# Kernel tuning notes

Hardware: AMD Instinct MI355X
Metric: run time of the kernel (lower is better)

Reference implementation:

```python
import jax, jax.numpy as jnp
import numpy as np

INV_SQRT3 = 0.5773502691896258  # e3nn wigner_3j entries for (0,1,1),(1,0,1),(1,1,0)


def setup_inputs() -> dict:
    key = jax.random.key(0)
    ks = jax.random.split(key, 9)
    B, N = 2, 256
    d_in, m1 = 256, 1          # input irreps: d_in x0e + m1 x1o
    d_h, m5, m3 = 256, 5, 3    # hidden irreps: d_h x0e + 5 x1o + 3 x1o
    d_out = 2                  # output irreps: 2 x0e
    return {
        "vectors": jax.random.normal(ks[0], (B, N, 3 * m1), jnp.float32),
        "scalars": jax.random.normal(ks[1], (B, N, d_in), jnp.float32),
        # e3nn internal weights ~ N(0,1); one weight block per CG path (uvw)
        "W1": jax.random.normal(ks[2], (d_in, d_in, d_h), jnp.float32),   # 0e x 0e -> 0e
        "W2a": jax.random.normal(ks[3], (d_in, m1, m5), jnp.float32),     # 0e x 1o -> 1o (mul 5)
        "W2b": jax.random.normal(ks[4], (d_in, m1, m3), jnp.float32),     # 0e x 1o -> 1o (mul 3)
        "W3a": jax.random.normal(ks[5], (m1, d_in, m5), jnp.float32),     # 1o x 0e -> 1o (mul 5)
        "W3b": jax.random.normal(ks[6], (m1, d_in, m3), jnp.float32),     # 1o x 0e -> 1o (mul 3)
        "W4": jax.random.normal(ks[7], (m1, m1, d_h), jnp.float32),       # 1o x 1o -> 0e
        "WL": jax.random.normal(ks[8], (d_h, d_out), jnp.float32),        # Linear d_h x0e -> 2 x0e
    }


def reference(vectors, scalars, W1, W2a, W2b, W3a, W3b, W4, WL):
    B, N, d = scalars.shape
    m1 = vectors.shape[-1] // 3
    z = B * N
    s = scalars.reshape(z, d)          # (z, d)  scalar (0e) channels
    v = vectors.reshape(z, m1, 3)      # (z, m1, 3)  vector (1o) channels
    d_h = W1.shape[-1]
    # e3nn FullyConnectedTensorProduct path weights ('component' irrep norm,
    # 'element' path norm): sqrt(ir_out.dim / sum_paths(mul1*mul2))
    pw0 = (1.0 / (d * d + m1 * m1)) ** 0.5      # into 0e output (paths 0e*0e and 1o*1o)
    pw1 = (3.0 / (2.0 * d * m1)) ** 0.5         # into each 1o output (paths 0e*1o and 1o*0e)
    # --- 0e x 0e -> 0e (dominant path) + 1o x 1o -> 0e ---
    t = jnp.einsum('zu,uvw->zvw', s, W1)        # (z, d, d_h)
    out0 = jnp.einsum('zv,zvw->zw', s, t)       # (z, d_h)
    out0 = out0 + INV_SQRT3 * jnp.einsum('zui,zvi,uvw->zw', v, v, W4)
    out0 = pw0 * out0
    # --- 0e x 1o -> 1o and 1o x 0e -> 1o (present in hidden irreps; they have
    # no path into the final 2x0e output, kept for structural fidelity) ---
    out1 = pw1 * INV_SQRT3 * (jnp.einsum('zu,zvk,uvw->zwk', s, v, W2a)
                              + jnp.einsum('zuk,zv,uvw->zwk', v, s, W3a))  # (z,5,3)
    out2 = pw1 * INV_SQRT3 * (jnp.einsum('zu,zvk,uvw->zwk', s, v, W2b)
                              + jnp.einsum('zuk,zv,uvw->zwk', v, s, W3b))  # (z,3,3)
    del out1, out2
    # --- e3nn Linear(hidden, 2x0e): only 0e->0e path, 1/sqrt(fan_in) norm ---
    lin = jnp.einsum('zu,uw->zw', out0, WL) / (d_h ** 0.5)   # (z, 2)
    m_eqv = lin[:, :1].reshape(B, N, 1)
    m_inv = lin[:, 1:].reshape(B, N, 1)
    return (m_eqv, m_inv)
```

## Files before the change

### kernel.cpp

```cpp
#include <hip/hip_runtime.h>


typedef __attribute__((ext_vector_type(8))) _Float16 f16x8;
typedef __attribute__((ext_vector_type(2))) _Float16 f16x2;
typedef __attribute__((ext_vector_type(4))) float f32x4;
typedef __attribute__((ext_vector_type(2))) int int2v;
typedef __attribute__((ext_vector_type(4))) int int4v;

#define LDS_S 32768
#define BP 80
#define BSTEP 5120
#define LDS_TOTAL (LDS_S + 4 * BSTEP)

__device__ __forceinline__ unsigned pkrtz(float a, float b) {
  return __builtin_bit_cast(unsigned, __builtin_amdgcn_cvt_pkrtz(a, b));
}
__device__ __forceinline__ int hbits(f16x2 h) {
  return __builtin_bit_cast(int, h);
}
__device__ __forceinline__ void barrier_lds() {
  asm volatile("s_waitcnt lgkmcnt(0)" ::: "memory");
  __builtin_amdgcn_s_barrier();
}

__global__ __launch_bounds__(256, 3) void eg_gemm(const float* __restrict__ s,
                                                  const float* __restrict__ W1,
                                                  float* __restrict__ out0) {
  extern __shared__ char smem[];
  char* sB = smem + LDS_S;

  const int bx = blockIdx.x;
  const int zh = bx >> 8;
  const int uvw = bx & 255;
  const int wt = uvw & 3, vc = (uvw >> 2) & 7, uc = uvw >> 5;
  const int u0 = uc * 32, v0 = vc * 32, w0 = wt * 64;

  const int t = threadIdx.x;
  const int lane = t & 63;
  const int wid = t >> 6;
  const int l15 = lane & 15;
  const int g = lane >> 4;

  for (int j = 0; j < 16; ++j) {
    int id = j * 256 + t;
    int zl = id >> 4;
    int c4 = id & 15;
    int srccol = (c4 < 8) ? (u0 + (c4 << 2)) : (v0 + ((c4 - 8) << 2));
    const float4 f = *(const float4*)(s + (zh * 256 + zl) * 256 + srccol);
    int slot = c4 >> 1;
    char* dst = smem + zl * 128 + (((slot ^ (zl & 7)) << 4) | ((c4 & 1) << 3));
    *(int2v*)dst = int2v{(int)pkrtz(f.x, f.y), (int)pkrtz(f.z, f.w)};
  }

  const int wB = t & 63;
  const int vg = t >> 6;
  const int hsw = (wB >> 3) & 7;
  const int sl0 = (vg ^ hsw) << 3;
  const int sl1 = ((vg + 4) ^ hsw) << 3;
  const float* gB = W1 + (size_t)u0 * 65536 + (v0 + vg * 4) * 256 + w0 + wB;

  float pa0, pa1, pa2, pa3, pa4, pa5, pa6, pa7;
  float pb0, pb1, pb2, pb3, pb4, pb5, pb6, pb7;

#define ISSUE(usbase)                                                       \
  do {                                                                      \
    const float* q0_ = gB + (size_t)(usbase) * 65536;                       \
    pa0 = q0_[0];    pa1 = q0_[256];      pa2 = q0_[512];  pa3 = q0_[768];  \
    pa4 = q0_[4096]; pa5 = q0_[4096+256]; pa6 = q0_[4096+512];              \
    pa7 = q0_[4096+768];                                                    \
    const float* q1_ = q0_ + 65536;                                         \
    pb0 = q1_[0];    pb1 = q1_[256];      pb2 = q1_[512];  pb3 = q1_[768];  \
    pb4 = q1_[4096]; pb5 = q1_[4096+256]; pb6 = q1_[4096+512];              \
    pb7 = q1_[4096+768];                                                    \
  } while (0)

#define WRITEPF(dst0_)                                                       \
  do {                                                                       \
    char* d0_ = (dst0_);                                                     \
    *(int2v*)(d0_ + wB * BP + sl0) =                                         \
        int2v{(int)pkrtz(pa0, pa1), (int)pkrtz(pa2, pa3)};                   \
    *(int2v*)(d0_ + wB * BP + sl1) =                                         \
        int2v{(int)pkrtz(pa4, pa5), (int)pkrtz(pa6, pa7)};                   \
    char* d1_ = d0_ + BSTEP;                                                 \
    *(int2v*)(d1_ + wB * BP + sl0) =                                         \
        int2v{(int)pkrtz(pb0, pb1), (int)pkrtz(pb2, pb3)};                   \
    *(int2v*)(d1_ + wB * BP + sl1) =                                         \
        int2v{(int)pkrtz(pb4, pb5), (int)pkrtz(pb6, pb7)};                   \
  } while (0)

  ISSUE(0);
  WRITEPF(sB);
  ISSUE(2);
  barrier_lds();

  const int swz = l15 & 7;
  int4v sv[4];
#pragma unroll
  for (int mf = 0; mf < 4; ++mf) {
    const char* p = smem + (wid * 64 + mf * 16 + l15) * 128 + (((4 + g) ^ swz) << 4);
    sv[mf] = *(const int4v*)p;
  }

  int baddr[4];
#pragma unroll
  for (int nf = 0; nf < 4; ++nf) {
    int w = nf * 16 + l15;
    baddr[nf] = w * BP + (((2 * g) ^ ((w >> 3) & 7)) << 3);
  }

  f32x4 acc[4][4];
#pragma unroll
  for (int a = 0; a < 4; ++a)
#pragma unroll
    for (int b = 0; b < 4; ++b) acc[a][b] = 0.f;

  for (int q = 0; q < 8; ++q) {
    int2v sur[4];
#pragma unroll
    for (int mf = 0; mf < 4; ++mf) {
      const char* p = smem + (wid * 64 + mf * 16 + l15) * 128 +
                      ((((q >> 1) ^ swz) << 4) | ((q & 1) << 3));
      sur[mf] = *(const int2v*)p;
    }
#pragma unroll
    for (int rr = 0; rr < 2; ++rr) {
      const int r = 2 * q + rr;
      const char* bufc = sB + rr * (2 * BSTEP);
      char* bufn = sB + (rr ^ 1) * (2 * BSTEP);
#pragma unroll
      for (int p = 0; p < 2; ++p) {
        f16x8 afr[4];
#pragma unroll
        for (int mf = 0; mf < 4; ++mf) {
          unsigned dw = (unsigned)sur[mf][rr];
          unsigned s2 = __builtin_amdgcn_perm(dw, dw, p ? 0x03020302u : 0x01000100u);
          f16x2 su2 = __builtin_bit_cast(f16x2, s2);
          int4v af;
#pragma unroll
          for (int jj = 0; jj < 4; ++jj) {
            f16x2 pv = __builtin_bit_cast(f16x2, (unsigned)sv[mf][jj]);
            f16x2 pr = su2 * pv;
            af[jj] = hbits(pr);
          }
          afr[mf] = __builtin_bit_cast(f16x8, af);
        }
        const char* bp = bufc + p * BSTEP;
#pragma unroll
        for (int nf = 0; nf < 4; ++nf) {
          int2v d0 = *(const int2v*)(bp + baddr[nf]);
          int2v d1 = *(const int2v*)(bp + (baddr[nf] ^ 8));
          int4v bf4 = int4v{d0[0], d0[1], d1[0], d1[1]};
          f16x8 bfr = __builtin_bit_cast(f16x8, bf4);
#pragma unroll
          for (int mf = 0; mf < 4; ++mf)
            acc[mf][nf] =
                __builtin_amdgcn_mfma_f32_16x16x32_f16(afr[mf], bfr, acc[mf][nf], 0, 0, 0);
        }
      }
      if (r < 15) WRITEPF(bufn);
      if (r < 14) ISSUE(2 * (r + 2));
      if (r < 15) barrier_lds();
    }
  }

#pragma unroll
  for (int mf = 0; mf < 4; ++mf)
#pragma unroll
    for (int nf = 0; nf < 4; ++nf)
#pragma unroll
      for (int rI = 0; rI < 4; ++rI) {
        int z = zh * 256 + wid * 64 + mf * 16 + g * 4 + rI;
        int w = w0 + nf * 16 + l15;
        atomicAdd(out0 + z * 256 + w, acc[mf][nf][rI]);
      }
}

__global__ void eg_finish(const float* __restrict__ vec,
                          const float* __restrict__ W4,
                          const float* __restrict__ WL,
                          const float* __restrict__ acc,
                          float* __restrict__ out) {
  const int z = blockIdx.x;
  const int lane = threadIdx.x;
  float v0 = vec[z * 3 + 0], v1 = vec[z * 3 + 1], v2 = vec[z * 3 + 2];
  const float b = 0.57735026918962576f * (v0 * v0 + v1 * v1 + v2 * v2);
  float a0 = 0.f, a1 = 0.f;
#pragma unroll
  for (int j = 0; j < 4; ++j) {
    int w = j * 64 + lane;
    float o = acc[z * 256 + w] + b * W4[w];
    a0 += o * WL[2 * w];
    a1 += o * WL[2 * w + 1];
  }
#pragma unroll
  for (int off = 32; off > 0; off >>= 1) {
    a0 += __shfl_xor(a0, off);
    a1 += __shfl_xor(a1, off);
  }
  if (lane == 0) {
    out[z] = 2.4413876e-04f * a0;
    out[512 + z] = 2.4413876e-04f * a1;
  }
}

extern "C" void kernel_launch(void* const* d_in, const int* in_sizes, int n_in,
                              void* d_out, int out_size, void* d_ws, size_t ws_size,
                              hipStream_t stream) {
  const float* vectors = (const float*)d_in[0];
  const float* scalars = (const float*)d_in[1];
  const float* W1 = (const float*)d_in[2];
  const float* W4 = (const float*)d_in[7];
  const float* WL = (const float*)d_in[8];
  float* out = (float*)d_out;
  float* acc = (float*)d_ws;

  (void)hipMemsetAsync(acc, 0, 512 * 256 * sizeof(float), stream);
  eg_gemm<<<512, 256, LDS_TOTAL, stream>>>(scalars, W1, acc);
  eg_finish<<<512, 64, 0, stream>>>(vectors, W4, WL, acc, out);
}
```

Baseline: 166.7 us.

## Halve z tile per block, deepen W1 prefetch, and stagger atomic columns

Each block now covers 128 z rows instead of 256, so the grid doubles to 1024 blocks, the scalar LDS tile halves, and launch bounds ask for 4 blocks per CU. The aim is more parallelism and occupancy. The W1 register prefetch moves from one stage ahead to two, using two alternating register buffers to hide global load latency better. The atomic epilogue rotates the column order per block to spread contention on the output. In exchange, every W1 tile is loaded twice (once per z half), so W1 global traffic doubles, and register pressure rises from the extra prefetch buffer.

```diff
diff --git a/kernel.cpp b/kernel.cpp
--- a/kernel.cpp
+++ b/kernel.cpp
@@ -7,7 +7,7 @@
 typedef __attribute__((ext_vector_type(2))) int int2v;
 typedef __attribute__((ext_vector_type(4))) int int4v;
 
-#define LDS_S 32768
+#define LDS_S 16384
 #define BP 80
 #define BSTEP 5120
 #define LDS_TOTAL (LDS_S + 4 * BSTEP)
@@ -23,7 +23,7 @@
   __builtin_amdgcn_s_barrier();
 }
 
-__global__ __launch_bounds__(256, 3) void eg_gemm(const float* __restrict__ s,
+__global__ __launch_bounds__(256, 4) void eg_gemm(const float* __restrict__ s,
                                                   const float* __restrict__ W1,
                                                   float* __restrict__ out0) {
   extern __shared__ char smem[];
@@ -41,12 +41,12 @@
   const int l15 = lane & 15;
   const int g = lane >> 4;
 
-  for (int j = 0; j < 16; ++j) {
+  for (int j = 0; j < 8; ++j) {
     int id = j * 256 + t;
     int zl = id >> 4;
     int c4 = id & 15;
     int srccol = (c4 < 8) ? (u0 + (c4 << 2)) : (v0 + ((c4 - 8) << 2));
-    const float4 f = *(const float4*)(s + (zh * 256 + zl) * 256 + srccol);
+    const float4 f = *(const float4*)(s + (zh * 128 + zl) * 256 + srccol);
     int slot = c4 >> 1;
     char* dst = smem + zl * 128 + (((slot ^ (zl & 7)) << 4) | ((c4 & 1) << 3));
     *(int2v*)dst = int2v{(int)pkrtz(f.x, f.y), (int)pkrtz(f.z, f.w)};
@@ -59,45 +59,47 @@
   const int sl1 = ((vg + 4) ^ hsw) << 3;
   const float* gB = W1 + (size_t)u0 * 65536 + (v0 + vg * 4) * 256 + w0 + wB;
 
-  float pa0, pa1, pa2, pa3, pa4, pa5, pa6, pa7;
-  float pb0, pb1, pb2, pb3, pb4, pb5, pb6, pb7;
-
-#define ISSUE(usbase)                                                       \
+  float pf0[16], pf1[16];
+
+#define ISSUE_TO(dst, usbase)                                               \
   do {                                                                      \
     const float* q0_ = gB + (size_t)(usbase) * 65536;                       \
-    pa0 = q0_[0];    pa1 = q0_[256];      pa2 = q0_[512];  pa3 = q0_[768];  \
-    pa4 = q0_[4096]; pa5 = q0_[4096+256]; pa6 = q0_[4096+512];              \
-    pa7 = q0_[4096+768];                                                    \
+    dst[0] = q0_[0];          dst[1] = q0_[256];                            \
+    dst[2] = q0_[512];        dst[3] = q0_[768];                            \
+    dst[4] = q0_[4096];       dst[5] = q0_[4096 + 256];                     \
+    dst[6] = q0_[4096 + 512]; dst[7] = q0_[4096 + 768];                     \
     const float* q1_ = q0_ + 65536;                                         \
-    pb0 = q1_[0];    pb1 = q1_[256];      pb2 = q1_[512];  pb3 = q1_[768];  \
-    pb4 = q1_[4096]; pb5 = q1_[4096+256]; pb6 = q1_[4096+512];              \
-    pb7 = q1_[4096+768];                                                    \
+    dst[8] = q1_[0];           dst[9] = q1_[256];                           \
+    dst[10] = q1_[512];        dst[11] = q1_[768];                          \
+    dst[12] = q1_[4096];       dst[13] = q1_[4096 + 256];                   \
+    dst[14] = q1_[4096 + 512]; dst[15] = q1_[4096 + 768];                   \
   } while (0)
 
-#define WRITEPF(dst0_)                                                       \
-  do {                                                                       \
-    char* d0_ = (dst0_);                                                     \
-    *(int2v*)(d0_ + wB * BP + sl0) =                                         \
-        int2v{(int)pkrtz(pa0, pa1), (int)pkrtz(pa2, pa3)};                   \
-    *(int2v*)(d0_ + wB * BP + sl1) =                                         \
-        int2v{(int)pkrtz(pa4, pa5), (int)pkrtz(pa6, pa7)};                   \
-    char* d1_ = d0_ + BSTEP;                                                 \
-    *(int2v*)(d1_ + wB * BP + sl0) =                                         \
-        int2v{(int)pkrtz(pb0, pb1), (int)pkrtz(pb2, pb3)};                   \
-    *(int2v*)(d1_ + wB * BP + sl1) =                                         \
-        int2v{(int)pkrtz(pb4, pb5), (int)pkrtz(pb6, pb7)};                   \
+#define WRITE_FROM(src, dst0_)                                              \
+  do {                                                                      \
+    char* d0_ = (dst0_);                                                    \
+    *(int2v*)(d0_ + wB * BP + sl0) =                                        \
+        int2v{(int)pkrtz(src[0], src[1]), (int)pkrtz(src[2], src[3])};      \
+    *(int2v*)(d0_ + wB * BP + sl1) =                                        \
+        int2v{(int)pkrtz(src[4], src[5]), (int)pkrtz(src[6], src[7])};      \
+    char* d1_ = d0_ + BSTEP;                                                \
+    *(int2v*)(d1_ + wB * BP + sl0) =                                        \
+        int2v{(int)pkrtz(src[8], src[9]), (int)pkrtz(src[10], src[11])};    \
+    *(int2v*)(d1_ + wB * BP + sl1) =                                        \
+        int2v{(int)pkrtz(src[12], src[13]), (int)pkrtz(src[14], src[15])};  \
   } while (0)
 
-  ISSUE(0);
-  WRITEPF(sB);
-  ISSUE(2);
+  ISSUE_TO(pf0, 0);
+  WRITE_FROM(pf0, sB);
+  ISSUE_TO(pf0, 2);
+  ISSUE_TO(pf1, 4);
   barrier_lds();
 
   const int swz = l15 & 7;
-  int4v sv[4];
-#pragma unroll
-  for (int mf = 0; mf < 4; ++mf) {
-    const char* p = smem + (wid * 64 + mf * 16 + l15) * 128 + (((4 + g) ^ swz) << 4);
+  int4v sv[2];
+#pragma unroll
+  for (int mf = 0; mf < 2; ++mf) {
+    const char* p = smem + (wid * 32 + mf * 16 + l15) * 128 + (((4 + g) ^ swz) << 4);
     sv[mf] = *(const int4v*)p;
   }
 
@@ -108,17 +110,17 @@
     baddr[nf] = w * BP + (((2 * g) ^ ((w >> 3) & 7)) << 3);
   }
 
-  f32x4 acc[4][4];
-#pragma unroll
-  for (int a = 0; a < 4; ++a)
+  f32x4 acc[2][4];
+#pragma unroll
+  for (int a = 0; a < 2; ++a)
 #pragma unroll
     for (int b = 0; b < 4; ++b) acc[a][b] = 0.f;
 
   for (int q = 0; q < 8; ++q) {
-    int2v sur[4];
-#pragma unroll
-    for (int mf = 0; mf < 4; ++mf) {
-      const char* p = smem + (wid * 64 + mf * 16 + l15) * 128 +
+    int2v sur[2];
+#pragma unroll
+    for (int mf = 0; mf < 2; ++mf) {
+      const char* p = smem + (wid * 32 + mf * 16 + l15) * 128 +
                       ((((q >> 1) ^ swz) << 4) | ((q & 1) << 3));
       sur[mf] = *(const int2v*)p;
     }
@@ -129,9 +131,9 @@
       char* bufn = sB + (rr ^ 1) * (2 * BSTEP);
 #pragma unroll
       for (int p = 0; p < 2; ++p) {
-        f16x8 afr[4];
-#pragma unroll
-        for (int mf = 0; mf < 4; ++mf) {
+        f16x8 afr[2];
+#pragma unroll
+        for (int mf = 0; mf < 2; ++mf) {
           unsigned dw = (unsigned)sur[mf][rr];
           unsigned s2 = __builtin_amdgcn_perm(dw, dw, p ? 0x03020302u : 0x01000100u);
           f16x2 su2 = __builtin_bit_cast(f16x2, s2);
@@ -152,27 +154,34 @@
           int4v bf4 = int4v{d0[0], d0[1], d1[0], d1[1]};
           f16x8 bfr = __builtin_bit_cast(f16x8, bf4);
 #pragma unroll
-          for (int mf = 0; mf < 4; ++mf)
+          for (int mf = 0; mf < 2; ++mf)
             acc[mf][nf] =
                 __builtin_amdgcn_mfma_f32_16x16x32_f16(afr[mf], bfr, acc[mf][nf], 0, 0, 0);
         }
       }
-      if (r < 15) WRITEPF(bufn);
-      if (r < 14) ISSUE(2 * (r + 2));
+      if (r < 15) {
+        if (rr == 0) WRITE_FROM(pf0, bufn); else WRITE_FROM(pf1, bufn);
+      }
+      if (r <= 12) {
+        if (rr == 0) ISSUE_TO(pf0, 2 * (r + 3)); else ISSUE_TO(pf1, 2 * (r + 3));
+      }
       if (r < 15) barrier_lds();
     }
   }
 
-#pragma unroll
-  for (int mf = 0; mf < 4; ++mf)
-#pragma unroll
-    for (int nf = 0; nf < 4; ++nf)
+  const int rot = (uc ^ vc) & 3;
+#pragma unroll
+  for (int mf = 0; mf < 2; ++mf)
+#pragma unroll
+    for (int nf = 0; nf < 4; ++nf) {
+      const int nfr = (nf + rot) & 3;
 #pragma unroll
       for (int rI = 0; rI < 4; ++rI) {
-        int z = zh * 256 + wid * 64 + mf * 16 + g * 4 + rI;
-        int w = w0 + nf * 16 + l15;
-        atomicAdd(out0 + z * 256 + w, acc[mf][nf][rI]);
-      }
+        int z = zh * 128 + wid * 32 + mf * 16 + g * 4 + rI;
+        int w = w0 + nfr * 16 + l15;
+        atomicAdd(out0 + z * 256 + w, acc[mf][nfr][rI]);
+      }
+    }
 }
 
 __global__ void eg_finish(const float* __restrict__ vec,
@@ -215,6 +224,6 @@
   float* acc = (float*)d_ws;
 
   (void)hipMemsetAsync(acc, 0, 512 * 256 * sizeof(float), stream);
-  eg_gemm<<<512, 256, LDS_TOTAL, stream>>>(scalars, W1, acc);
+  eg_gemm<<<1024, 256, LDS_TOTAL, stream>>>(scalars, W1, acc);
   eg_finish<<<512, 64, 0, stream>>>(vectors, W4, WL, acc, out);
 }
```

Measured after the change: 177.9 us. 6.7% more time.
